# Kernel tuning notes

Measured on AMD Instinct MI355X. Metric: run time of the kernel, lower is better.

Reference implementation:

```python
import jax, jax.numpy as jnp
import numpy as np
from jax import lax

KS = 7; KC = 64; S = 31; B = 1; H = 128; W = 128; ITERS = 3
LAM = 0.1   # Softshrink lambda
EPS = 1e-5  # BatchNorm eps


def conv2d(x, w, b):
    # x: [N,C,H,W], w: [O,C,kh,kw], b: [O]; stride 1, SAME padding (ks odd)
    y = lax.conv_general_dilated(x, w, (1, 1), 'SAME',
                                 dimension_numbers=('NCHW', 'OIHW', 'NCHW'))
    return y + b[None, :, None, None]


def band_conv(x5, w, b):
    # x5: [S,B,C,H,W] -> apply shared conv per band by merging S into batch
    s, bb, c, h, ww = x5.shape
    y = conv2d(x5.reshape(s * bb, c, h, ww), w, b)
    return y.reshape(s, bb, -1, h, ww)


def softshrink(x):
    return jnp.sign(x) * jnp.maximum(jnp.abs(x) - LAM, 0.0)


def setup_inputs() -> dict:
    key = jax.random.key(0)
    ks = jax.random.split(key, 12)
    sc = 0.05
    inputs = jax.random.normal(ks[0], (B, S, H, W), jnp.float32)
    W_fe   = jax.random.normal(ks[1], (KC, 1, KS, KS), jnp.float32) * sc
    b_fe   = jax.random.normal(ks[2], (KC,), jnp.float32) * sc
    W_enc  = jax.random.normal(ks[3], (ITERS, KC, 1, KS, KS), jnp.float32) * sc
    b_enc  = jax.random.normal(ks[4], (ITERS, KC), jnp.float32) * sc
    W_dec  = jax.random.normal(ks[5], (ITERS, 1, KC, KS, KS), jnp.float32) * sc
    b_dec  = jax.random.normal(ks[6], (ITERS, 1), jnp.float32) * sc
    W_last = jax.random.normal(ks[7], (1, KC, KS, KS), jnp.float32) * sc
    b_last = jax.random.normal(ks[8], (1,), jnp.float32) * sc
    W_z    = jax.random.normal(ks[9], (ITERS, KC, KC, KS, KS), jnp.float32) * sc
    b_z    = jax.random.normal(ks[10], (ITERS, KC), jnp.float32) * sc
    bn_gamma = jnp.ones((ITERS, KC), jnp.float32)
    bn_beta  = jnp.zeros((ITERS, KC), jnp.float32)
    return dict(inputs=inputs, W_fe=W_fe, b_fe=b_fe, W_enc=W_enc, b_enc=b_enc,
                W_dec=W_dec, b_dec=b_dec, W_last=W_last, b_last=b_last,
                W_z=W_z, b_z=b_z, bn_gamma=bn_gamma, bn_beta=bn_beta)


def reference(inputs, W_fe, b_fe, W_enc, b_enc, W_dec, b_dec,
              W_last, b_last, W_z, b_z, bn_gamma, bn_beta):
    # inputs: [B, S, H, W]; treat each band as [B,1,H,W]
    x = jnp.transpose(inputs, (1, 0, 2, 3))[:, :, None]  # [S,B,1,H,W]
    # initial sparse code per band (shared first encoder + softshrink)
    csc = softshrink(band_conv(x, W_fe, b_fe))            # [S,B,KC,H,W]

    for it in range(ITERS):
        lyr = it % ITERS  # cycle(range(_layers)) with _layers == ista_iters
        # per-band ISTA step (vectorized over bands)
        res = x - band_conv(csc, W_dec[lyr], b_dec[lyr])
        tmp = softshrink(csc + band_conv(res, W_enc[lyr], b_enc[lyr]))
        # GRU-style gate: sigmoid(BN(conv(tmp))); BN uses per-call (per-band)
        # batch statistics over (B,H,W) per channel, matching training mode
        zpre = band_conv(tmp, W_z[lyr], b_z[lyr])          # [S,B,KC,H,W]
        mu = jnp.mean(zpre, axis=(1, 3, 4), keepdims=True)
        var = jnp.var(zpre, axis=(1, 3, 4), keepdims=True)
        zn = (zpre - mu) * lax.rsqrt(var + EPS)
        g = bn_gamma[lyr][None, None, :, None, None]
        be = bn_beta[lyr][None, None, :, None, None]
        z = jax.nn.sigmoid(zn * g + be)
        # direction alternates: even iters sweep bands forward, odd backward
        fwd = (it % 2 == 0)
        t = tmp if fwd else tmp[::-1]
        zz = z if fwd else z[::-1]

        def step(carry, inp):
            ti, zi = inp
            new = zi * carry + (1.0 - zi) * ti
            return new, new

        _, ys = lax.scan(step, t[0], (t[1:], zz[1:]))
        seq = jnp.concatenate([t[:1], ys], axis=0)
        csc = seq if fwd else seq[::-1]

    out = band_conv(csc, W_last, b_last)[:, :, 0]  # [S,B,H,W]
    outputs = jnp.transpose(out, (1, 0, 2, 3))     # [B,S,H,W]
    return (csc, outputs)
```

## Files before the change

### kernel.cpp

```cpp
#include <hip/hip_runtime.h>
#include <hip/hip_bf16.h>
#include <math.h>

#define S31   31
#define KC    64
#define KS    7
#define KK    49
#define IMG   128
#define HW    16384
#define LAM   0.1f
#define BNEPS 1e-5f

#define PLSTRIDE 3872

#define TW    32
#define TH    8
#define DTW   38
#define DTH   14
#define DTILE 532

typedef __attribute__((ext_vector_type(8))) short  frag8;
typedef __attribute__((ext_vector_type(4))) float  facc4;

static __device__ __forceinline__ short f2bf(float f) {
    union { float f; unsigned u; } x; x.f = f;
    unsigned r = x.u + 0x7fffu + ((x.u >> 16) & 1u);
    return (short)(r >> 16);
}

__global__ void reorder_weights(const float* __restrict__ Wz,
                                const float* __restrict__ Wenc,
                                const float* __restrict__ Wfe,
                                short* __restrict__ wz_frag,
                                float* __restrict__ wenc_r,
                                float* __restrict__ wfe_r,
                                float* __restrict__ pstats) {
    int tid = blockIdx.x * 256 + threadIdx.x;
    const int NZ = 3 * KK * 4096;
    const int NE = 3 * KK * KC;
    const int NF = KK * KC;
    const int NP = 2 * S31 * KC;
    if (tid < NZ) {
        int j    = tid & 7;
        int lane = (tid >> 3) & 63;
        int og   = (tid >> 9) & 3;
        int ks   = (tid >> 11) & 1;
        int rem  = tid >> 12;
        int khkw = rem % KK;
        int lyr  = rem / KK;
        int ic = ks * 32 + ((lane >> 4) << 3) + j;
        int oc = (og << 4) + (lane & 15);
        float w = Wz[(((size_t)lyr * KC + oc) * KC + ic) * KK + khkw];
        wz_frag[tid] = f2bf(w);
    } else if (tid < NZ + NE) {
        int t = tid - NZ;
        int oc = t & 63;
        int kk = t >> 6;
        int k  = kk % KK;
        int lyr = kk / KK;
        wenc_r[t] = Wenc[((size_t)lyr * KC + oc) * KK + k];
    } else if (tid < NZ + NE + NF) {
        int t = tid - NZ - NE;
        int oc = t & 63;
        int k  = t >> 6;
        wfe_r[t] = Wfe[oc * KK + k];
    } else if (tid < NZ + NE + NF + NP) {
        pstats[tid - NZ - NE - NF] = 0.f;
    }
}

__global__ __launch_bounds__(256) void conv1to64(
        const float* __restrict__ src,
        const float* __restrict__ wr,
        const float* __restrict__ bias,
        const float* __restrict__ addsrc,
        float* __restrict__ dst,
        short* __restrict__ dst_t)
{
    int s    = blockIdx.y;
    int half = blockIdx.x & 1;
    int tile = blockIdx.x >> 1;
    int t    = threadIdx.x;
    int tx = t & 31, ty = t >> 5;
    int w0 = (tile & 3) << 5, h0 = (tile >> 2) << 3;

    __shared__ float t_s[DTILE];
    const float* sp = src + (size_t)s * HW;
    for (int i = threadIdx.x; i < DTILE; i += 256) {
        int r = i / DTW, c = i - r * DTW;
        int hh = h0 - 3 + r, ww = w0 - 3 + c;
        t_s[i] = (hh >= 0 && hh < IMG && ww >= 0 && ww < IMG) ? sp[hh * IMG + ww] : 0.f;
    }
    __syncthreads();

    int pix = (h0 + ty) * IMG + (w0 + tx);
    size_t base = ((size_t)s * KC + half * 32) * HW + pix;

    float addv[32];
    if (addsrc) {
#pragma unroll
        for (int i = 0; i < 32; i++) addv[i] = addsrc[base + (size_t)i * HW];
    } else {
#pragma unroll
        for (int i = 0; i < 32; i++) addv[i] = 0.f;
    }
    __builtin_amdgcn_sched_barrier(0);

    float acc[32];
#pragma unroll
    for (int i = 0; i < 32; i++) acc[i] = 0.f;

    const float* wrh = wr + half * 32;
#pragma unroll 1
    for (int kh = 0; kh < KS; kh++) {
#pragma unroll
        for (int kw = 0; kw < KS; kw++) {
            float v = t_s[(ty + kh) * DTW + tx + kw];
            const float* wk = wrh + (kh * KS + kw) * KC;
#pragma unroll
            for (int i = 0; i < 32; i++) acc[i] += v * wk[i];
        }
    }

#pragma unroll
    for (int g = 0; g < 4; g++) {
        frag8 vv;
#pragma unroll
        for (int j = 0; j < 8; j++) {
            int i = g * 8 + j;
            float v = acc[i] + bias[half * 32 + i];
            v += addv[i];
            v = (v > LAM) ? (v - LAM) : ((v < -LAM) ? (v + LAM) : 0.f);
            dst[base + (size_t)i * HW] = v;
            vv[j] = f2bf(v);
        }
        if (dst_t) {
            *(frag8*)(dst_t + ((size_t)s * HW + pix) * KC + half * 32 + g * 8) = vv;
        }
    }
}

#define ICB   4
#define CHUNK (ICB * DTILE)

__global__ __launch_bounds__(256) void conv64to1(
        const float* __restrict__ src,
        const float* __restrict__ w,
        const float* __restrict__ bias,
        const float* __restrict__ xsub,
        float* __restrict__ dst)
{
    int s    = blockIdx.y;
    int tile = blockIdx.x;
    int tx = threadIdx.x & 31, ty = threadIdx.x >> 5;
    int w0 = (tile & 3) << 5, h0 = (tile >> 2) << 3;

    __shared__ float t_s[2][CHUNK];

    int  goff[9];
    bool okf[9];
#pragma unroll
    for (int r = 0; r < 9; r++) {
        int j = threadIdx.x + r * 256;
        if (j < CHUNK) {
            int plane = j / DTILE, p = j - plane * DTILE;
            int rr = p / DTW, cc = p - rr * DTW;
            int hh = h0 - 3 + rr, ww = w0 - 3 + cc;
            bool inb = (hh >= 0 && hh < IMG && ww >= 0 && ww < IMG);
            goff[r] = plane * HW + (inb ? (hh * IMG + ww) : 0);
            okf[r]  = inb;
        }
    }

    const float* sbase = src + (size_t)s * KC * HW;

    float ldv[9];
#pragma unroll
    for (int r = 0; r < 9; r++)
        if (threadIdx.x + r * 256 < CHUNK)
            ldv[r] = okf[r] ? sbase[goff[r]] : 0.f;
#pragma unroll
    for (int r = 0; r < 9; r++)
        if (threadIdx.x + r * 256 < CHUNK)
            t_s[0][threadIdx.x + r * 256] = ldv[r];

    float acc = 0.f;
    __syncthreads();

#pragma unroll 1
    for (int blk = 0; blk < 16; blk++) {
        int cur = blk & 1;
        if (blk < 15) {
            const float* nb = sbase + (size_t)(blk + 1) * ICB * HW;
#pragma unroll
            for (int r = 0; r < 9; r++)
                if (threadIdx.x + r * 256 < CHUNK)
                    ldv[r] = okf[r] ? nb[goff[r]] : 0.f;
        }
        __builtin_amdgcn_sched_barrier(0);
#pragma unroll
        for (int pl = 0; pl < ICB; pl++) {
            int ic = blk * ICB + pl;
            const float* wk = w + ic * KK;
            const float* ts = &t_s[cur][pl * DTILE];
#pragma unroll 1
            for (int kh = 0; kh < KS; kh++) {
#pragma unroll
                for (int kw = 0; kw < KS; kw++)
                    acc += ts[(ty + kh) * DTW + tx + kw] * wk[kh * KS + kw];
            }
        }
        __syncthreads();
        if (blk < 15) {
#pragma unroll
            for (int r = 0; r < 9; r++)
                if (threadIdx.x + r * 256 < CHUNK)
                    t_s[cur ^ 1][threadIdx.x + r * 256] = ldv[r];
            __syncthreads();
        }
    }

    float v = acc + bias[0];
    int pix = (h0 + ty) * IMG + (w0 + tx);
    if (xsub) v = xsub[(size_t)s * HW + pix] - v;
    dst[(size_t)s * HW + pix] = v;
}

__global__ __launch_bounds__(256, 4) void conv_z_mfma(
        const short* __restrict__ srcT,
        const short* __restrict__ wfrag,
        const float* __restrict__ bias,
        float* __restrict__ dst,
        float* __restrict__ pstats)
{
    __shared__ __align__(16) short a_s[4 * PLSTRIDE];

    int s    = blockIdx.y;
    int tile = blockIdx.x;
    int h0 = (tile >> 3) << 4, w0 = (tile & 7) << 4;
    int tid  = threadIdx.x;
    int wave = tid >> 6, lane = tid & 63;
    int q = lane >> 4, m = lane & 15;

    const short* tsrc = srcT + (size_t)s * HW * KC;

    facc4 acc[4][4];
#pragma unroll
    for (int i = 0; i < 4; i++)
#pragma unroll
        for (int j = 0; j < 4; j++)
            acc[i][j] = (facc4){0.f, 0.f, 0.f, 0.f};

#pragma unroll 1
    for (int pass = 0; pass < 2; ++pass) {
        if (pass) __syncthreads();

#pragma unroll
        for (int rep = 0; rep < 2; rep++) {
            int p = tid + rep * 256;
            if (p < 484) {
                int r = p / 22, c = p - r * 22;
                int hh = h0 - 3 + r, ww = w0 - 3 + c;
                bool ok = (hh >= 0 && hh < IMG && ww >= 0 && ww < IMG);
                const short* px = tsrc + ((size_t)(ok ? (hh * IMG + ww) : 0) << 6)
                                       + (pass << 5);
                short* dp = a_s + p * 8;
#pragma unroll
                for (int c4 = 0; c4 < 4; c4++) {
                    frag8 v;
                    if (ok) v = *(const frag8*)(px + (c4 << 3));
                    else    v = (frag8)(short)0;
                    *(frag8*)(dp + c4 * PLSTRIDE) = v;
                }
            }
        }
        __syncthreads();

        const short* arow = a_s + q * PLSTRIDE + (wave * 4 * 22 + m) * 8;
        const frag8* brow = (const frag8*)wfrag + (pass * 4) * 64 + lane;

#pragma unroll 1
        for (int kh = 0; kh < 7; ++kh) {
#pragma unroll
            for (int kw = 0; kw < 7; ++kw) {
                frag8 b0 = brow[kw * 512 + 0 * 64];
                frag8 b1 = brow[kw * 512 + 1 * 64];
                frag8 b2 = brow[kw * 512 + 2 * 64];
                frag8 b3 = brow[kw * 512 + 3 * 64];
                frag8 a0 = *(const frag8*)(arow + (0 * 22 + kw) * 8);
                frag8 a1 = *(const frag8*)(arow + (1 * 22 + kw) * 8);
                frag8 a2 = *(const frag8*)(arow + (2 * 22 + kw) * 8);
                frag8 a3 = *(const frag8*)(arow + (3 * 22 + kw) * 8);
                acc[0][0] = __builtin_amdgcn_mfma_f32_16x16x32_bf16(a0, b0, acc[0][0], 0, 0, 0);
                acc[0][1] = __builtin_amdgcn_mfma_f32_16x16x32_bf16(a0, b1, acc[0][1], 0, 0, 0);
                acc[0][2] = __builtin_amdgcn_mfma_f32_16x16x32_bf16(a0, b2, acc[0][2], 0, 0, 0);
                acc[0][3] = __builtin_amdgcn_mfma_f32_16x16x32_bf16(a0, b3, acc[0][3], 0, 0, 0);
                acc[1][0] = __builtin_amdgcn_mfma_f32_16x16x32_bf16(a1, b0, acc[1][0], 0, 0, 0);
                acc[1][1] = __builtin_amdgcn_mfma_f32_16x16x32_bf16(a1, b1, acc[1][1], 0, 0, 0);
                acc[1][2] = __builtin_amdgcn_mfma_f32_16x16x32_bf16(a1, b2, acc[1][2], 0, 0, 0);
                acc[1][3] = __builtin_amdgcn_mfma_f32_16x16x32_bf16(a1, b3, acc[1][3], 0, 0, 0);
                acc[2][0] = __builtin_amdgcn_mfma_f32_16x16x32_bf16(a2, b0, acc[2][0], 0, 0, 0);
                acc[2][1] = __builtin_amdgcn_mfma_f32_16x16x32_bf16(a2, b1, acc[2][1], 0, 0, 0);
                acc[2][2] = __builtin_amdgcn_mfma_f32_16x16x32_bf16(a2, b2, acc[2][2], 0, 0, 0);
                acc[2][3] = __builtin_amdgcn_mfma_f32_16x16x32_bf16(a2, b3, acc[2][3], 0, 0, 0);
                acc[3][0] = __builtin_amdgcn_mfma_f32_16x16x32_bf16(a3, b0, acc[3][0], 0, 0, 0);
                acc[3][1] = __builtin_amdgcn_mfma_f32_16x16x32_bf16(a3, b1, acc[3][1], 0, 0, 0);
                acc[3][2] = __builtin_amdgcn_mfma_f32_16x16x32_bf16(a3, b2, acc[3][2], 0, 0, 0);
                acc[3][3] = __builtin_amdgcn_mfma_f32_16x16x32_bf16(a3, b3, acc[3][3], 0, 0, 0);
            }
            arow += 22 * 8;
            brow += 7 * 512;
        }
    }

    int prow = h0 + wave * 4;
#pragma unroll
    for (int og = 0; og < 4; og++) {
        int oc = og * 16 + m;
        float bb = bias[oc];
        float s1 = 0.f, s2 = 0.f;
#pragma unroll
        for (int pg = 0; pg < 4; pg++) {
            float* dp = dst + ((size_t)s * KC + oc) * HW
                            + (size_t)(prow + pg) * IMG + w0 + q * 4;
            float4 v;
            v.x = acc[pg][og][0] + bb;
            v.y = acc[pg][og][1] + bb;
            v.z = acc[pg][og][2] + bb;
            v.w = acc[pg][og][3] + bb;
            s1 += v.x + v.y + v.z + v.w;
            s2 += v.x * v.x + v.y * v.y + v.z * v.z + v.w * v.w;
            *(float4*)dp = v;
        }
        s1 += __shfl_xor(s1, 16, 64); s2 += __shfl_xor(s2, 16, 64);
        s1 += __shfl_xor(s1, 32, 64); s2 += __shfl_xor(s2, 32, 64);
        if (q == 0) {
            atomicAdd(&pstats[(s * KC + oc) * 2],     s1);
            atomicAdd(&pstats[(s * KC + oc) * 2 + 1], s2);
        }
    }
}

__global__ __launch_bounds__(64) void bn_finalize(
        float* __restrict__ pstats,
        float* __restrict__ stats)
{
    int i = blockIdx.x * 64 + threadIdx.x;
    if (i < S31 * KC) {
        float s1 = pstats[i * 2], s2 = pstats[i * 2 + 1];
        pstats[i * 2] = 0.f;
        pstats[i * 2 + 1] = 0.f;
        float mu  = s1 * (1.f / HW);
        float var = s2 * (1.f / HW) - mu * mu;
        if (var < 0.f) var = 0.f;
        stats[i * 2]     = mu;
        stats[i * 2 + 1] = rsqrtf(var + BNEPS);
    }
}

__global__ __launch_bounds__(256) void band_scan(
        const float* __restrict__ tmp,
        const float* __restrict__ zpre,
        const float* __restrict__ stats,
        const float* __restrict__ gamma,
        const float* __restrict__ beta,
        float* __restrict__ csc,
        int fwd)
{
    int idx = blockIdx.x * 256 + threadIdx.x;
    int c = idx >> 14;
    float g = gamma[c], be = beta[c];
    float prev = 0.f;
    for (int step = 0; step < S31; step++) {
        int s = fwd ? step : (S31 - 1 - step);
        size_t off = (size_t)s * KC * HW + idx;
        float t  = tmp[off];
        float zp = zpre[off];
        float mu = stats[(s * KC + c) * 2];
        float rs = stats[(s * KC + c) * 2 + 1];
        float zn = (zp - mu) * rs * g + be;
        float z  = 1.f / (1.f + expf(-zn));
        float cur = (step == 0) ? t : (z * prev + (1.f - z) * t);
        csc[off] = cur;
        prev = cur;
    }
}

extern "C" void kernel_launch(void* const* d_in, const int* in_sizes, int n_in,
                              void* d_out, int out_size, void* d_ws, size_t ws_size,
                              hipStream_t stream) {
    const float* x      = (const float*)d_in[0];
    const float* W_fe   = (const float*)d_in[1];
    const float* b_fe   = (const float*)d_in[2];
    const float* W_enc  = (const float*)d_in[3];
    const float* b_enc  = (const float*)d_in[4];
    const float* W_dec  = (const float*)d_in[5];
    const float* b_dec  = (const float*)d_in[6];
    const float* W_last = (const float*)d_in[7];
    const float* b_last = (const float*)d_in[8];
    const float* W_z    = (const float*)d_in[9];
    const float* b_z    = (const float*)d_in[10];
    const float* bn_g   = (const float*)d_in[11];
    const float* bn_b   = (const float*)d_in[12];

    float* out     = (float*)d_out;
    float* csc     = out;
    float* outputs = out + (size_t)S31 * KC * HW;

    char* ws = (char*)d_ws;
    float* tmp     = (float*)ws; ws += (size_t)S31 * KC * HW * 4;
    float* zpre    = (float*)ws; ws += (size_t)S31 * KC * HW * 4;
    float* res     = (float*)ws; ws += (size_t)S31 * HW * 4;
    float* stats   = (float*)ws; ws += (size_t)S31 * KC * 2 * 4;
    float* pstats  = (float*)ws; ws += (size_t)S31 * KC * 2 * 4;
    short* wz_frag = (short*)ws; ws += (size_t)3 * KK * 4096 * 2;
    float* wenc_r  = (float*)ws; ws += (size_t)3 * KK * KC * 4;
    float* wfe_r   = (float*)ws; ws += (size_t)KK * KC * 4;
    short* tmp_t   = (short*)ws; ws += (size_t)S31 * HW * KC * 2;

    {
        int total = 3 * KK * 4096 + 3 * KK * KC + KK * KC + 2 * S31 * KC;
        reorder_weights<<<(total + 255) / 256, 256, 0, stream>>>(
            W_z, W_enc, W_fe, wz_frag, wenc_r, wfe_r, pstats);
    }

    dim3 gconv(64, S31);
    dim3 gconv2(128, S31);

    conv1to64<<<gconv2, 256, 0, stream>>>(x, wfe_r, b_fe, nullptr, csc, nullptr);

    for (int it = 0; it < 3; it++) {
        int lyr = it;
        conv64to1<<<gconv, 256, 0, stream>>>(
            csc, W_dec + (size_t)lyr * KC * KK, b_dec + lyr, x, res);
        conv1to64<<<gconv2, 256, 0, stream>>>(
            res, wenc_r + (size_t)lyr * KK * KC, b_enc + (size_t)lyr * KC, csc,
            tmp, tmp_t);
        conv_z_mfma<<<gconv, 256, 0, stream>>>(
            tmp_t, wz_frag + (size_t)lyr * KK * 4096, b_z + (size_t)lyr * KC,
            zpre, pstats);
        bn_finalize<<<S31, 64, 0, stream>>>(pstats, stats);
        band_scan<<<(KC * HW) / 256, 256, 0, stream>>>(
            tmp, zpre, stats, bn_g + (size_t)lyr * KC, bn_b + (size_t)lyr * KC,
            csc, (it % 2 == 0) ? 1 : 0);
    }

    conv64to1<<<gconv, 256, 0, stream>>>(csc, W_last, b_last, nullptr, outputs);
}
```

Baseline: 1.811 ms.

## Split conv_z across 8 waves, prefetch weight fragments, split channel-halves layout

The z-gate MFMA conv now launches 512 threads per block, so each wave handles 2 pixel rows instead of 4, halving the accumulator count per thread. Weight B-fragments are software-prefetched one kw step ahead into registers, and the bf16 transposed activation buffer is split into two contiguous 32-channel halves so each pass reads a dense plane. The aim is more waves in flight to hide LDS and global latency. The cost is more register pressure from the prefetch, and a padded weight buffer to absorb the last-step overread.

```diff
diff --git a/kernel.cpp b/kernel.cpp
--- a/kernel.cpp
+++ b/kernel.cpp
@@ -122,6 +122,7 @@
         }
     }
 
+    short* tb = dst_t ? (dst_t + (((size_t)half * S31 + s) * HW + pix) * 32) : nullptr;
 #pragma unroll
     for (int g = 0; g < 4; g++) {
         frag8 vv;
@@ -134,9 +135,7 @@
             dst[base + (size_t)i * HW] = v;
             vv[j] = f2bf(v);
         }
-        if (dst_t) {
-            *(frag8*)(dst_t + ((size_t)s * HW + pix) * KC + half * 32 + g * 8) = vv;
-        }
+        if (tb) *(frag8*)(tb + g * 8) = vv;
     }
 }
 
@@ -226,7 +225,7 @@
     dst[(size_t)s * HW + pix] = v;
 }
 
-__global__ __launch_bounds__(256, 4) void conv_z_mfma(
+__global__ __launch_bounds__(512, 4) void conv_z_mfma(
         const short* __restrict__ srcT,
         const short* __restrict__ wfrag,
         const float* __restrict__ bias,
@@ -242,11 +241,9 @@
     int wave = tid >> 6, lane = tid & 63;
     int q = lane >> 4, m = lane & 15;
 
-    const short* tsrc = srcT + (size_t)s * HW * KC;
-
-    facc4 acc[4][4];
-#pragma unroll
-    for (int i = 0; i < 4; i++)
+    facc4 acc[2][4];
+#pragma unroll
+    for (int i = 0; i < 2; i++)
 #pragma unroll
         for (int j = 0; j < 4; j++)
             acc[i][j] = (facc4){0.f, 0.f, 0.f, 0.f};
@@ -255,15 +252,17 @@
     for (int pass = 0; pass < 2; ++pass) {
         if (pass) __syncthreads();
 
-#pragma unroll
-        for (int rep = 0; rep < 2; rep++) {
-            int p = tid + rep * 256;
+        const frag8* brow = (const frag8*)wfrag + (pass * 4) * 64 + lane;
+        frag8 c0 = brow[0], c1 = brow[64], c2 = brow[128], c3 = brow[192];
+
+        const short* tsrc = srcT + ((size_t)pass * S31 + s) * HW * 32;
+        {
+            int p = tid;
             if (p < 484) {
                 int r = p / 22, c = p - r * 22;
                 int hh = h0 - 3 + r, ww = w0 - 3 + c;
                 bool ok = (hh >= 0 && hh < IMG && ww >= 0 && ww < IMG);
-                const short* px = tsrc + ((size_t)(ok ? (hh * IMG + ww) : 0) << 6)
-                                       + (pass << 5);
+                const short* px = tsrc + (size_t)(ok ? (hh * IMG + ww) : 0) * 32;
                 short* dp = a_s + p * 8;
 #pragma unroll
                 for (int c4 = 0; c4 < 4; c4++) {
@@ -276,51 +275,39 @@
         }
         __syncthreads();
 
-        const short* arow = a_s + q * PLSTRIDE + (wave * 4 * 22 + m) * 8;
-        const frag8* brow = (const frag8*)wfrag + (pass * 4) * 64 + lane;
+        const short* arow = a_s + q * PLSTRIDE + (wave * 2 * 22 + m) * 8;
 
 #pragma unroll 1
         for (int kh = 0; kh < 7; ++kh) {
 #pragma unroll
             for (int kw = 0; kw < 7; ++kw) {
-                frag8 b0 = brow[kw * 512 + 0 * 64];
-                frag8 b1 = brow[kw * 512 + 1 * 64];
-                frag8 b2 = brow[kw * 512 + 2 * 64];
-                frag8 b3 = brow[kw * 512 + 3 * 64];
+                const frag8* bn = brow + (kw == 6 ? 7 : (kw + 1)) * 512;
+                frag8 n0 = bn[0], n1 = bn[64], n2 = bn[128], n3 = bn[192];
                 frag8 a0 = *(const frag8*)(arow + (0 * 22 + kw) * 8);
                 frag8 a1 = *(const frag8*)(arow + (1 * 22 + kw) * 8);
-                frag8 a2 = *(const frag8*)(arow + (2 * 22 + kw) * 8);
-                frag8 a3 = *(const frag8*)(arow + (3 * 22 + kw) * 8);
-                acc[0][0] = __builtin_amdgcn_mfma_f32_16x16x32_bf16(a0, b0, acc[0][0], 0, 0, 0);
-                acc[0][1] = __builtin_amdgcn_mfma_f32_16x16x32_bf16(a0, b1, acc[0][1], 0, 0, 0);
-                acc[0][2] = __builtin_amdgcn_mfma_f32_16x16x32_bf16(a0, b2, acc[0][2], 0, 0, 0);
-                acc[0][3] = __builtin_amdgcn_mfma_f32_16x16x32_bf16(a0, b3, acc[0][3], 0, 0, 0);
-                acc[1][0] = __builtin_amdgcn_mfma_f32_16x16x32_bf16(a1, b0, acc[1][0], 0, 0, 0);
-                acc[1][1] = __builtin_amdgcn_mfma_f32_16x16x32_bf16(a1, b1, acc[1][1], 0, 0, 0);
-                acc[1][2] = __builtin_amdgcn_mfma_f32_16x16x32_bf16(a1, b2, acc[1][2], 0, 0, 0);
-                acc[1][3] = __builtin_amdgcn_mfma_f32_16x16x32_bf16(a1, b3, acc[1][3], 0, 0, 0);
-                acc[2][0] = __builtin_amdgcn_mfma_f32_16x16x32_bf16(a2, b0, acc[2][0], 0, 0, 0);
-                acc[2][1] = __builtin_amdgcn_mfma_f32_16x16x32_bf16(a2, b1, acc[2][1], 0, 0, 0);
-                acc[2][2] = __builtin_amdgcn_mfma_f32_16x16x32_bf16(a2, b2, acc[2][2], 0, 0, 0);
-                acc[2][3] = __builtin_amdgcn_mfma_f32_16x16x32_bf16(a2, b3, acc[2][3], 0, 0, 0);
-                acc[3][0] = __builtin_amdgcn_mfma_f32_16x16x32_bf16(a3, b0, acc[3][0], 0, 0, 0);
-                acc[3][1] = __builtin_amdgcn_mfma_f32_16x16x32_bf16(a3, b1, acc[3][1], 0, 0, 0);
-                acc[3][2] = __builtin_amdgcn_mfma_f32_16x16x32_bf16(a3, b2, acc[3][2], 0, 0, 0);
-                acc[3][3] = __builtin_amdgcn_mfma_f32_16x16x32_bf16(a3, b3, acc[3][3], 0, 0, 0);
+                acc[0][0] = __builtin_amdgcn_mfma_f32_16x16x32_bf16(a0, c0, acc[0][0], 0, 0, 0);
+                acc[0][1] = __builtin_amdgcn_mfma_f32_16x16x32_bf16(a0, c1, acc[0][1], 0, 0, 0);
+                acc[0][2] = __builtin_amdgcn_mfma_f32_16x16x32_bf16(a0, c2, acc[0][2], 0, 0, 0);
+                acc[0][3] = __builtin_amdgcn_mfma_f32_16x16x32_bf16(a0, c3, acc[0][3], 0, 0, 0);
+                acc[1][0] = __builtin_amdgcn_mfma_f32_16x16x32_bf16(a1, c0, acc[1][0], 0, 0, 0);
+                acc[1][1] = __builtin_amdgcn_mfma_f32_16x16x32_bf16(a1, c1, acc[1][1], 0, 0, 0);
+                acc[1][2] = __builtin_amdgcn_mfma_f32_16x16x32_bf16(a1, c2, acc[1][2], 0, 0, 0);
+                acc[1][3] = __builtin_amdgcn_mfma_f32_16x16x32_bf16(a1, c3, acc[1][3], 0, 0, 0);
+                c0 = n0; c1 = n1; c2 = n2; c3 = n3;
             }
             arow += 22 * 8;
             brow += 7 * 512;
         }
     }
 
-    int prow = h0 + wave * 4;
+    int prow = h0 + wave * 2;
 #pragma unroll
     for (int og = 0; og < 4; og++) {
         int oc = og * 16 + m;
         float bb = bias[oc];
         float s1 = 0.f, s2 = 0.f;
 #pragma unroll
-        for (int pg = 0; pg < 4; pg++) {
+        for (int pg = 0; pg < 2; pg++) {
             float* dp = dst + ((size_t)s * KC + oc) * HW
                             + (size_t)(prow + pg) * IMG + w0 + q * 4;
             float4 v;
@@ -413,10 +400,10 @@
     float* res     = (float*)ws; ws += (size_t)S31 * HW * 4;
     float* stats   = (float*)ws; ws += (size_t)S31 * KC * 2 * 4;
     float* pstats  = (float*)ws; ws += (size_t)S31 * KC * 2 * 4;
-    short* wz_frag = (short*)ws; ws += (size_t)3 * KK * 4096 * 2;
+    short* wz_frag = (short*)ws; ws += ((size_t)3 * KK * 4096 + 4096) * 2;
     float* wenc_r  = (float*)ws; ws += (size_t)3 * KK * KC * 4;
     float* wfe_r   = (float*)ws; ws += (size_t)KK * KC * 4;
-    short* tmp_t   = (short*)ws; ws += (size_t)S31 * HW * KC * 2;
+    short* tmp_t   = (short*)ws; ws += (size_t)2 * S31 * HW * 32 * 2;
 
     {
         int total = 3 * KK * 4096 + 3 * KK * KC + KK * KC + 2 * S31 * KC;
@@ -436,7 +423,7 @@
         conv1to64<<<gconv2, 256, 0, stream>>>(
             res, wenc_r + (size_t)lyr * KK * KC, b_enc + (size_t)lyr * KC, csc,
             tmp, tmp_t);
-        conv_z_mfma<<<gconv, 256, 0, stream>>>(
+        conv_z_mfma<<<gconv, 512, 0, stream>>>(
             tmp_t, wz_frag + (size_t)lyr * KK * 4096, b_z + (size_t)lyr * KC,
             zpre, pstats);
         bn_finalize<<<S31, 64, 0, stream>>>(pstats, stats);
```

Result: slower. 2.053 ms (+13.4%).
